# Performance work log

Hardware: AMD Instinct MI355X
Metric: run time of the kernel (lower is better)

## Reference

```python
import jax, jax.numpy as jnp
import numpy as np

NEG_SLOPE = 0.2   # negative_slope
EPS = 1e-6        # leaky-relu eps
BN_EPS = 1e-5     # torch BatchNorm default eps


def setup_inputs() -> dict:
    key = jax.random.key(0)
    k1, k2, k3 = jax.random.split(key, 3)
    B, C_in, C_out, N = 8, 256, 256, 8192
    x = jax.random.normal(k1, (B, C_in, 3, N), dtype=jnp.float32)
    s = 1.0 / np.sqrt(C_in)  # nn.Linear default init range
    W_feat = jax.random.uniform(k2, (C_out, C_in), minval=-s, maxval=s, dtype=jnp.float32)
    W_dir = jax.random.uniform(k3, (C_out, C_in), minval=-s, maxval=s, dtype=jnp.float32)
    gamma = jnp.ones((C_out,), jnp.float32)
    beta = jnp.zeros((C_out,), jnp.float32)
    return {"x": x, "W_feat": W_feat, "W_dir": W_dir, "gamma": gamma, "beta": beta}


def reference(x, W_feat, W_dir, gamma, beta):
    # VNLinear: kron(W, eye(3)) conv2d == per-vector channel mix
    p = jnp.einsum('oc,bcdn->bodn', W_feat, x)  # [B, O, 3, N]

    # VNBatchNorm: BN (training mode, batch stats) on vector norms, then rescale
    norm = jnp.sqrt(jnp.sum(p * p, axis=2))           # [B, O, N]
    mean = jnp.mean(norm, axis=(0, 2))                # [O]
    var = jnp.var(norm, axis=(0, 2))                  # [O] biased, as torch BN
    norm_bn = ((norm - mean[None, :, None]) * jax.lax.rsqrt(var + BN_EPS)[None, :, None]
               * gamma[None, :, None] + beta[None, :, None])
    p = p / norm[:, :, None, :] * norm_bn[:, :, None, :]

    # VNLeakyReLU with direction computed from the ORIGINAL input x
    d = jnp.einsum('oc,bcdn->bodn', W_dir, x)         # [B, O, 3, N]
    dot = jnp.sum(p * d, axis=2, keepdims=True)       # [B, O, 1, N]
    d_norm_sq = jnp.sum(d * d, axis=2, keepdims=True)
    return jnp.where(dot >= 0, p, p - (1.0 - NEG_SLOPE) * (dot / (d_norm_sq + EPS)) * d)
```

## Files before the change

kernel.cpp:

```cpp
#include <hip/hip_runtime.h>
#include <math.h>

#define BDIM 8
#define CIN  256
#define COUT 256
#define NDIM 8192

#define NEG_COEF  0.8f
#define LRELU_EPS 1e-6f
#define BN_EPS    1e-5f

typedef __attribute__((ext_vector_type(8))) short bf16x8;
typedef __attribute__((ext_vector_type(4))) float f32x4;

#define WS_WFH 0
#define WS_WFL 65536
#define WS_WDH 131072
#define WS_WDL 196608
#define WS_STATS_BYTE 524288
#define NSLOT 8

__device__ __forceinline__ unsigned short f2bf(float f) {
    unsigned u = __float_as_uint(f);
    return (unsigned short)((u + 0x7FFFu + ((u >> 16) & 1u)) >> 16);
}
__device__ __forceinline__ float bf2f(unsigned short h) {
    return __uint_as_float(((unsigned)h) << 16);
}

__global__ __launch_bounds__(256) void setup_w_kernel(
    const float* __restrict__ Wf, const float* __restrict__ Wd,
    unsigned short* __restrict__ wsu)
{
    const int o = blockIdx.x;
    const int mat = blockIdx.y;
    const int c = threadIdx.x;
    const float* W = mat ? Wd : Wf;
    float w = W[o * CIN + c];
    unsigned short hi = f2bf(w);
    unsigned short lo = f2bf(w - bf2f(hi));
    int pos = (c & ~31) + 4 * (c & 7) + ((c >> 3) & 3);
    unsigned short* ph = wsu + (mat ? WS_WDH : WS_WFH);
    unsigned short* pl = wsu + (mat ? WS_WDL : WS_WFL);
    ph[o * CIN + pos] = hi;
    pl[o * CIN + pos] = lo;
}

__global__ __launch_bounds__(256) void vn_stats_mfma(
    const float* __restrict__ x, const unsigned short* __restrict__ wsu,
    float* __restrict__ stats)
{
    __shared__ unsigned short sXhi[192 * 40];
    __shared__ float redS[64], redQ[64];

    const int t  = threadIdx.x;
    const int n0 = blockIdx.x * 64;
    const int o0 = blockIdx.y * 64;
    const int b  = blockIdx.z;

    const int lane = t & 63;
    const int w    = t >> 6;
    const int q    = lane >> 4;
    const int ln   = lane & 15;

    const int jl = t & 31;
    const int kb = t >> 5;

    if (t < 64) { redS[t] = 0.f; redQ[t] = 0.f; }

    f32x4 acc[2][6];
    #pragma unroll
    for (int i = 0; i < 2; ++i)
        #pragma unroll
        for (int j = 0; j < 6; ++j) acc[i][j] = (f32x4)0.f;

    const unsigned short* wfh = wsu + WS_WFH;
    const int oo = o0 + (w >> 1) * 32;
    const int nb = (w & 1) * 32;

    for (int c0 = 0; c0 < CIN; c0 += 32) {
        __syncthreads();
        #pragma unroll
        for (int ip = 0; ip < 6; ++ip) {
            int jloc = ip * 32 + jl;
            int d = jloc >> 6, nl = jloc & 63;
            float v[4];
            #pragma unroll
            for (int i = 0; i < 4; ++i) {
                int c = c0 + kb + 8 * i;
                v[i] = x[((size_t)((b * CIN + c) * 3 + d)) * NDIM + n0 + nl];
            }
            unsigned p0 = (unsigned)f2bf(v[0]) | ((unsigned)f2bf(v[1]) << 16);
            unsigned p1 = (unsigned)f2bf(v[2]) | ((unsigned)f2bf(v[3]) << 16);
            *(uint2*)&sXhi[jloc * 40 + kb * 4] = make_uint2(p0, p1);
        }
        __syncthreads();
        bf16x8 af[2];
        #pragma unroll
        for (int mt = 0; mt < 2; ++mt)
            af[mt] = *(const bf16x8*)&wfh[(oo + mt * 16 + ln) * CIN + c0 + q * 8];
        #pragma unroll
        for (int nt = 0; nt < 6; ++nt) {
            int d = nt >> 1, h = nt & 1;
            int jloc = d * 64 + nb + h * 16 + ln;
            bf16x8 bh = *(const bf16x8*)&sXhi[jloc * 40 + q * 8];
            #pragma unroll
            for (int mt = 0; mt < 2; ++mt)
                acc[mt][nt] = __builtin_amdgcn_mfma_f32_16x16x32_bf16(af[mt], bh, acc[mt][nt], 0, 0, 0);
        }
    }

    #pragma unroll
    for (int mt = 0; mt < 2; ++mt) {
        #pragma unroll
        for (int r = 0; r < 4; ++r) {
            float s = 0.f, s2 = 0.f;
            #pragma unroll
            for (int h = 0; h < 2; ++h) {
                float p0 = acc[mt][0 + h][r];
                float p1 = acc[mt][2 + h][r];
                float p2 = acc[mt][4 + h][r];
                float n2 = p0 * p0 + p1 * p1 + p2 * p2;
                s += sqrtf(n2); s2 += n2;
            }
            #pragma unroll
            for (int m = 1; m < 16; m <<= 1) {
                s  += __shfl_xor(s,  m, 64);
                s2 += __shfl_xor(s2, m, 64);
            }
            if (ln == 0) {
                int ol = (w >> 1) * 32 + mt * 16 + q * 4 + r;
                atomicAdd(&redS[ol], s);
                atomicAdd(&redQ[ol], s2);
            }
        }
    }
    __syncthreads();
    if (t < 64) {
        int slot = blockIdx.x & (NSLOT - 1);
        atomicAdd(&stats[slot * 256 + o0 + t], redS[t]);
        atomicAdd(&stats[NSLOT * 256 + slot * 256 + o0 + t], redQ[t]);
    }
}

__global__ __launch_bounds__(256) void vn_finalize2(
    float* __restrict__ stats, const float* __restrict__ gamma)
{
    int o = threadIdx.x;
    float s = 0.f, s2 = 0.f;
    #pragma unroll
    for (int i = 0; i < NSLOT; ++i) {
        s  += stats[i * 256 + o];
        s2 += stats[(NSLOT + i) * 256 + o];
    }
    const float inv = 1.0f / (float)(BDIM * NDIM);
    float mean = s * inv;
    float var  = fmaxf(s2 * inv - mean * mean, 0.f);
    stats[2 * NSLOT * 256 + o] = mean;
    stats[2 * NSLOT * 256 + 256 + o] = gamma[o] * rsqrtf(var + BN_EPS);
}

__global__ __launch_bounds__(256) void vn_main_mfma(
    const float* __restrict__ x, const unsigned short* __restrict__ wsu,
    const float* __restrict__ stats, const float* __restrict__ beta,
    float* __restrict__ out)
{
    __shared__ unsigned short sXhi[192 * 40];
    __shared__ unsigned short sXlo[192 * 40];

    const int t  = threadIdx.x;
    const int n0 = blockIdx.x * 64;
    const int o0 = blockIdx.y * 64;
    const int b  = blockIdx.z;

    const int lane = t & 63;
    const int w    = t >> 6;
    const int q    = lane >> 4;
    const int ln   = lane & 15;

    const int jl = t & 31;
    const int kb = t >> 5;

    f32x4 accP[2][6], accD[2][6];
    #pragma unroll
    for (int i = 0; i < 2; ++i)
        #pragma unroll
        for (int j = 0; j < 6; ++j) { accP[i][j] = (f32x4)0.f; accD[i][j] = (f32x4)0.f; }

    const unsigned short* wfh = wsu + WS_WFH;
    const unsigned short* wfl = wsu + WS_WFL;
    const unsigned short* wdh = wsu + WS_WDH;
    const unsigned short* wdl = wsu + WS_WDL;
    const int oo = o0 + (w >> 1) * 32;
    const int nb = (w & 1) * 32;

    for (int c0 = 0; c0 < CIN; c0 += 32) {
        __syncthreads();
        #pragma unroll
        for (int ip = 0; ip < 6; ++ip) {
            int jloc = ip * 32 + jl;
            int d = jloc >> 6, nl = jloc & 63;
            float v[4];
            #pragma unroll
            for (int i = 0; i < 4; ++i) {
                int c = c0 + kb + 8 * i;
                v[i] = x[((size_t)((b * CIN + c) * 3 + d)) * NDIM + n0 + nl];
            }
            unsigned short h0 = f2bf(v[0]), h1 = f2bf(v[1]), h2 = f2bf(v[2]), h3 = f2bf(v[3]);
            unsigned ph0 = (unsigned)h0 | ((unsigned)h1 << 16);
            unsigned ph1 = (unsigned)h2 | ((unsigned)h3 << 16);
            unsigned pl0 = (unsigned)f2bf(v[0] - bf2f(h0)) | ((unsigned)f2bf(v[1] - bf2f(h1)) << 16);
            unsigned pl1 = (unsigned)f2bf(v[2] - bf2f(h2)) | ((unsigned)f2bf(v[3] - bf2f(h3)) << 16);
            *(uint2*)&sXhi[jloc * 40 + kb * 4] = make_uint2(ph0, ph1);
            *(uint2*)&sXlo[jloc * 40 + kb * 4] = make_uint2(pl0, pl1);
        }
        __syncthreads();
        bf16x8 afh[2], afl[2], adh[2], adl[2];
        #pragma unroll
        for (int mt = 0; mt < 2; ++mt) {
            int row = (oo + mt * 16 + ln) * CIN + c0 + q * 8;
            afh[mt] = *(const bf16x8*)&wfh[row];
            afl[mt] = *(const bf16x8*)&wfl[row];
            adh[mt] = *(const bf16x8*)&wdh[row];
            adl[mt] = *(const bf16x8*)&wdl[row];
        }
        #pragma unroll
        for (int nt = 0; nt < 6; ++nt) {
            int d = nt >> 1, h = nt & 1;
            int jloc = d * 64 + nb + h * 16 + ln;
            bf16x8 bh = *(const bf16x8*)&sXhi[jloc * 40 + q * 8];
            bf16x8 bl = *(const bf16x8*)&sXlo[jloc * 40 + q * 8];
            #pragma unroll
            for (int mt = 0; mt < 2; ++mt) {
                f32x4 aP = accP[mt][nt];
                aP = __builtin_amdgcn_mfma_f32_16x16x32_bf16(afh[mt], bh, aP, 0, 0, 0);
                aP = __builtin_amdgcn_mfma_f32_16x16x32_bf16(afh[mt], bl, aP, 0, 0, 0);
                aP = __builtin_amdgcn_mfma_f32_16x16x32_bf16(afl[mt], bh, aP, 0, 0, 0);
                aP = __builtin_amdgcn_mfma_f32_16x16x32_bf16(afl[mt], bl, aP, 0, 0, 0);
                accP[mt][nt] = aP;
                f32x4 aD = accD[mt][nt];
                aD = __builtin_amdgcn_mfma_f32_16x16x32_bf16(adh[mt], bh, aD, 0, 0, 0);
                aD = __builtin_amdgcn_mfma_f32_16x16x32_bf16(adh[mt], bl, aD, 0, 0, 0);
                aD = __builtin_amdgcn_mfma_f32_16x16x32_bf16(adl[mt], bh, aD, 0, 0, 0);
                accD[mt][nt] = aD;
            }
        }
    }

    const float* meanp  = stats + 2 * NSLOT * 256;
    const float* scalep = meanp + 256;
    #pragma unroll
    for (int mt = 0; mt < 2; ++mt) {
        #pragma unroll
        for (int r = 0; r < 4; ++r) {
            const int o = oo + mt * 16 + q * 4 + r;
            const float mean  = meanp[o];
            const float scale = scalep[o];
            const float bet   = beta[o];
            #pragma unroll
            for (int h = 0; h < 2; ++h) {
                float p0 = accP[mt][0 + h][r], p1 = accP[mt][2 + h][r], p2 = accP[mt][4 + h][r];
                float d0 = accD[mt][0 + h][r], d1 = accD[mt][2 + h][r], d2 = accD[mt][4 + h][r];
                float n2 = p0 * p0 + p1 * p1 + p2 * p2;
                float nr = sqrtf(n2);
                float f  = ((nr - mean) * scale + bet) / nr;
                p0 *= f; p1 *= f; p2 *= f;
                float dot = p0 * d0 + p1 * d1 + p2 * d2;
                if (dot < 0.f) {
                    float g = NEG_COEF * dot / (d0 * d0 + d1 * d1 + d2 * d2 + LRELU_EPS);
                    p0 -= g * d0; p1 -= g * d1; p2 -= g * d2;
                }
                const int n = n0 + nb + h * 16 + ln;
                out[((size_t)(b * COUT + o) * 3 + 0) * NDIM + n] = p0;
                out[((size_t)(b * COUT + o) * 3 + 1) * NDIM + n] = p1;
                out[((size_t)(b * COUT + o) * 3 + 2) * NDIM + n] = p2;
            }
        }
    }
}

extern "C" void kernel_launch(void* const* d_in, const int* in_sizes, int n_in,
                              void* d_out, int out_size, void* d_ws, size_t ws_size,
                              hipStream_t stream) {
    const float* x     = (const float*)d_in[0];
    const float* Wf    = (const float*)d_in[1];
    const float* Wd    = (const float*)d_in[2];
    const float* gamma = (const float*)d_in[3];
    const float* beta  = (const float*)d_in[4];
    float* out = (float*)d_out;
    unsigned short* wsu = (unsigned short*)d_ws;
    float* stats = (float*)((char*)d_ws + WS_STATS_BYTE);

    hipMemsetAsync((char*)d_ws + WS_STATS_BYTE, 0, 2 * NSLOT * 256 * sizeof(float), stream);

    setup_w_kernel<<<dim3(256, 2), 256, 0, stream>>>(Wf, Wd, wsu);
    dim3 grid(NDIM / 64, COUT / 64, BDIM);
    vn_stats_mfma<<<grid, 256, 0, stream>>>(x, wsu, stats);
    vn_finalize2<<<1, 256, 0, stream>>>(stats, gamma);
    vn_main_mfma<<<grid, 256, 0, stream>>>(x, wsu, stats, beta, out);
}
```

Baseline: 601.4 us.

## Pre-convert x to swizzled bf16 hi/lo tiles in stats pass, reuse in main

The stats kernel now covers all 256 output channels per block (512 threads), so each x tile is read from fp32 and split into bf16 hi/lo only once. The swizzled tiles are written to a workspace image. The main kernel then loads these pre-split tiles directly into LDS with global_load_lds instead of re-reading fp32 x and redoing the split per output block. This removes three of the four redundant x reads and conversions in the stats pass, and all of them in the main pass. In exchange it writes and reads about 200 MB of extra workspace, and it falls back to the old path when the workspace is too small.

```diff
diff --git a/kernel.cpp b/kernel.cpp
--- a/kernel.cpp
+++ b/kernel.cpp
@@ -19,6 +19,11 @@
 #define WS_WDL 196608
 #define WS_STATS_BYTE 524288
 #define NSLOT 8
+#define TILE_BYTES 12288
+#define WS_XHI_BYTE 557056
+#define XIMG_BYTES 100663296ull
+#define WS_XLO_BYTE (WS_XHI_BYTE + XIMG_BYTES)
+#define WS_NEED (WS_XLO_BYTE + XIMG_BYTES)
 
 __device__ __forceinline__ unsigned short f2bf(float f) {
     unsigned u = __float_as_uint(f);
@@ -26,6 +31,16 @@
 }
 __device__ __forceinline__ float bf2f(unsigned short h) {
     return __uint_as_float(((unsigned)h) << 16);
+}
+
+__device__ __forceinline__ int swz(int off) {
+    return off ^ (((off >> 6) & 7) << 4);
+}
+
+__device__ __forceinline__ void gl_lds16(const char* g, char* l) {
+    __builtin_amdgcn_global_load_lds(
+        (const __attribute__((address_space(1))) unsigned int*)g,
+        (__attribute__((address_space(3))) unsigned int*)l, 16, 0, 0);
 }
 
 __global__ __launch_bounds__(256) void setup_w_kernel(
@@ -46,17 +61,21 @@
     pl[o * CIN + pos] = lo;
 }
 
-__global__ __launch_bounds__(256) void vn_stats_mfma(
+__global__ __launch_bounds__(512) void vn_statscvt(
     const float* __restrict__ x, const unsigned short* __restrict__ wsu,
+    char* __restrict__ xh, char* __restrict__ xl,
     float* __restrict__ stats)
 {
-    __shared__ unsigned short sXhi[192 * 40];
-    __shared__ float redS[64], redQ[64];
-
-    const int t  = threadIdx.x;
-    const int n0 = blockIdx.x * 64;
-    const int o0 = blockIdx.y * 64;
-    const int b  = blockIdx.z;
+    __shared__ uint4 sH4[TILE_BYTES / 16];
+    __shared__ uint4 sL4[TILE_BYTES / 16];
+    __shared__ float redS[256], redQ[256];
+    char* sH = (char*)sH4;
+    char* sL = (char*)sL4;
+
+    const int t    = threadIdx.x;
+    const int nblk = blockIdx.x;
+    const int b    = blockIdx.z;
+    const int n0   = nblk * 64;
 
     const int lane = t & 63;
     const int w    = t >> 6;
@@ -64,46 +83,64 @@
     const int ln   = lane & 15;
 
     const int jl = t & 31;
-    const int kb = t >> 5;
-
-    if (t < 64) { redS[t] = 0.f; redQ[t] = 0.f; }
-
-    f32x4 acc[2][6];
+    const int kb = (t >> 5) & 7;
+    const int u  = t >> 8;
+
+    if (t < 256) { redS[t] = 0.f; redQ[t] = 0.f; }
+
+    f32x4 acc[2][12];
     #pragma unroll
     for (int i = 0; i < 2; ++i)
         #pragma unroll
-        for (int j = 0; j < 6; ++j) acc[i][j] = (f32x4)0.f;
+        for (int j = 0; j < 12; ++j) acc[i][j] = (f32x4)0.f;
 
     const unsigned short* wfh = wsu + WS_WFH;
-    const int oo = o0 + (w >> 1) * 32;
-    const int nb = (w & 1) * 32;
-
-    for (int c0 = 0; c0 < CIN; c0 += 32) {
-        __syncthreads();
-        #pragma unroll
-        for (int ip = 0; ip < 6; ++ip) {
-            int jloc = ip * 32 + jl;
-            int d = jloc >> 6, nl = jloc & 63;
+    const int oo = w * 32;
+    char* ghb = xh + ((size_t)(b * 128 + nblk)) * (8 * TILE_BYTES);
+    char* glb = xl + ((size_t)(b * 128 + nblk)) * (8 * TILE_BYTES);
+
+    for (int ct = 0; ct < 8; ++ct) {
+        const int c0 = ct * 32;
+        __syncthreads();
+        #pragma unroll
+        for (int s = 0; s < 3; ++s) {
+            const int ip = u * 3 + s;
+            const int jloc = ip * 32 + jl;
+            const int d = jloc >> 6, nl = jloc & 63;
             float v[4];
             #pragma unroll
             for (int i = 0; i < 4; ++i) {
                 int c = c0 + kb + 8 * i;
                 v[i] = x[((size_t)((b * CIN + c) * 3 + d)) * NDIM + n0 + nl];
             }
-            unsigned p0 = (unsigned)f2bf(v[0]) | ((unsigned)f2bf(v[1]) << 16);
-            unsigned p1 = (unsigned)f2bf(v[2]) | ((unsigned)f2bf(v[3]) << 16);
-            *(uint2*)&sXhi[jloc * 40 + kb * 4] = make_uint2(p0, p1);
-        }
-        __syncthreads();
+            unsigned short h0 = f2bf(v[0]), h1 = f2bf(v[1]), h2 = f2bf(v[2]), h3 = f2bf(v[3]);
+            uint2 ph = make_uint2((unsigned)h0 | ((unsigned)h1 << 16),
+                                  (unsigned)h2 | ((unsigned)h3 << 16));
+            uint2 pl = make_uint2(
+                (unsigned)f2bf(v[0] - bf2f(h0)) | ((unsigned)f2bf(v[1] - bf2f(h1)) << 16),
+                (unsigned)f2bf(v[2] - bf2f(h2)) | ((unsigned)f2bf(v[3] - bf2f(h3)) << 16));
+            const int off = swz(jloc * 64 + kb * 8);
+            *(uint2*)(sH + off) = ph;
+            *(uint2*)(sL + off) = pl;
+        }
+        __syncthreads();
+        {
+            const int off = t * 48;
+            const char* src = (off < TILE_BYTES) ? (sH + off) : (sL + off - TILE_BYTES);
+            char* dst = (off < TILE_BYTES) ? (ghb + ct * TILE_BYTES + off)
+                                           : (glb + ct * TILE_BYTES + off - TILE_BYTES);
+            #pragma unroll
+            for (int p = 0; p < 3; ++p)
+                *(uint4*)(dst + p * 16) = *(const uint4*)(src + p * 16);
+        }
         bf16x8 af[2];
         #pragma unroll
         for (int mt = 0; mt < 2; ++mt)
             af[mt] = *(const bf16x8*)&wfh[(oo + mt * 16 + ln) * CIN + c0 + q * 8];
         #pragma unroll
-        for (int nt = 0; nt < 6; ++nt) {
-            int d = nt >> 1, h = nt & 1;
-            int jloc = d * 64 + nb + h * 16 + ln;
-            bf16x8 bh = *(const bf16x8*)&sXhi[jloc * 40 + q * 8];
+        for (int nt = 0; nt < 12; ++nt) {
+            const int jloc = nt * 16 + ln;
+            bf16x8 bh = *(const bf16x8*)(sH + swz(jloc * 64 + q * 16));
             #pragma unroll
             for (int mt = 0; mt < 2; ++mt)
                 acc[mt][nt] = __builtin_amdgcn_mfma_f32_16x16x32_bf16(af[mt], bh, acc[mt][nt], 0, 0, 0);
@@ -116,10 +153,10 @@
         for (int r = 0; r < 4; ++r) {
             float s = 0.f, s2 = 0.f;
             #pragma unroll
-            for (int h = 0; h < 2; ++h) {
+            for (int h = 0; h < 4; ++h) {
                 float p0 = acc[mt][0 + h][r];
-                float p1 = acc[mt][2 + h][r];
-                float p2 = acc[mt][4 + h][r];
+                float p1 = acc[mt][4 + h][r];
+                float p2 = acc[mt][8 + h][r];
                 float n2 = p0 * p0 + p1 * p1 + p2 * p2;
                 s += sqrtf(n2); s2 += n2;
             }
@@ -129,17 +166,17 @@
                 s2 += __shfl_xor(s2, m, 64);
             }
             if (ln == 0) {
-                int ol = (w >> 1) * 32 + mt * 16 + q * 4 + r;
-                atomicAdd(&redS[ol], s);
-                atomicAdd(&redQ[ol], s2);
+                int o = oo + mt * 16 + q * 4 + r;
+                atomicAdd(&redS[o], s);
+                atomicAdd(&redQ[o], s2);
             }
         }
     }
     __syncthreads();
-    if (t < 64) {
-        int slot = blockIdx.x & (NSLOT - 1);
-        atomicAdd(&stats[slot * 256 + o0 + t], redS[t]);
-        atomicAdd(&stats[NSLOT * 256 + slot * 256 + o0 + t], redQ[t]);
+    if (t < 256) {
+        int slot = nblk & (NSLOT - 1);
+        atomicAdd(&stats[slot * 256 + t], redS[t]);
+        atomicAdd(&stats[NSLOT * 256 + slot * 256 + t], redQ[t]);
     }
 }
 
@@ -160,26 +197,27 @@
     stats[2 * NSLOT * 256 + 256 + o] = gamma[o] * rsqrtf(var + BN_EPS);
 }
 
-__global__ __launch_bounds__(256) void vn_main_mfma(
-    const float* __restrict__ x, const unsigned short* __restrict__ wsu,
+__global__ __launch_bounds__(256) void vn_main2(
+    const unsigned short* __restrict__ wsu,
+    const char* __restrict__ xh, const char* __restrict__ xl,
     const float* __restrict__ stats, const float* __restrict__ beta,
     float* __restrict__ out)
 {
-    __shared__ unsigned short sXhi[192 * 40];
-    __shared__ unsigned short sXlo[192 * 40];
-
-    const int t  = threadIdx.x;
-    const int n0 = blockIdx.x * 64;
-    const int o0 = blockIdx.y * 64;
-    const int b  = blockIdx.z;
+    __shared__ uint4 sH4[TILE_BYTES / 16];
+    __shared__ uint4 sL4[TILE_BYTES / 16];
+    char* sH = (char*)sH4;
+    char* sL = (char*)sL4;
+
+    const int t    = threadIdx.x;
+    const int nblk = blockIdx.x;
+    const int n0   = nblk * 64;
+    const int o0   = blockIdx.y * 64;
+    const int b    = blockIdx.z;
 
     const int lane = t & 63;
     const int w    = t >> 6;
     const int q    = lane >> 4;
     const int ln   = lane & 15;
-
-    const int jl = t & 31;
-    const int kb = t >> 5;
 
     f32x4 accP[2][6], accD[2][6];
     #pragma unroll
@@ -194,31 +232,23 @@
     const int oo = o0 + (w >> 1) * 32;
     const int nb = (w & 1) * 32;
 
-    for (int c0 = 0; c0 < CIN; c0 += 32) {
-        __syncthreads();
-        #pragma unroll
-        for (int ip = 0; ip < 6; ++ip) {
-            int jloc = ip * 32 + jl;
-            int d = jloc >> 6, nl = jloc & 63;
-            float v[4];
-            #pragma unroll
-            for (int i = 0; i < 4; ++i) {
-                int c = c0 + kb + 8 * i;
-                v[i] = x[((size_t)((b * CIN + c) * 3 + d)) * NDIM + n0 + nl];
-            }
-            unsigned short h0 = f2bf(v[0]), h1 = f2bf(v[1]), h2 = f2bf(v[2]), h3 = f2bf(v[3]);
-            unsigned ph0 = (unsigned)h0 | ((unsigned)h1 << 16);
-            unsigned ph1 = (unsigned)h2 | ((unsigned)h3 << 16);
-            unsigned pl0 = (unsigned)f2bf(v[0] - bf2f(h0)) | ((unsigned)f2bf(v[1] - bf2f(h1)) << 16);
-            unsigned pl1 = (unsigned)f2bf(v[2] - bf2f(h2)) | ((unsigned)f2bf(v[3] - bf2f(h3)) << 16);
-            *(uint2*)&sXhi[jloc * 40 + kb * 4] = make_uint2(ph0, ph1);
-            *(uint2*)&sXlo[jloc * 40 + kb * 4] = make_uint2(pl0, pl1);
-        }
-        __syncthreads();
+    const char* ghb = xh + ((size_t)(b * 128 + nblk)) * (8 * TILE_BYTES);
+    const char* glb = xl + ((size_t)(b * 128 + nblk)) * (8 * TILE_BYTES);
+
+    for (int ct = 0; ct < 8; ++ct) {
+        __syncthreads();
+        #pragma unroll
+        for (int p = 0; p < 3; ++p) {
+            gl_lds16(ghb + ct * TILE_BYTES + t * 16 + p * 4096, sH + t * 16 + p * 4096);
+            gl_lds16(glb + ct * TILE_BYTES + t * 16 + p * 4096, sL + t * 16 + p * 4096);
+        }
+        __syncthreads();
+
+        const int c0 = ct * 32;
         bf16x8 afh[2], afl[2], adh[2], adl[2];
         #pragma unroll
         for (int mt = 0; mt < 2; ++mt) {
-            int row = (oo + mt * 16 + ln) * CIN + c0 + q * 8;
+            const int row = (oo + mt * 16 + ln) * CIN + c0 + q * 8;
             afh[mt] = *(const bf16x8*)&wfh[row];
             afl[mt] = *(const bf16x8*)&wfl[row];
             adh[mt] = *(const bf16x8*)&wdh[row];
@@ -226,10 +256,11 @@
         }
         #pragma unroll
         for (int nt = 0; nt < 6; ++nt) {
-            int d = nt >> 1, h = nt & 1;
-            int jloc = d * 64 + nb + h * 16 + ln;
-            bf16x8 bh = *(const bf16x8*)&sXhi[jloc * 40 + q * 8];
-            bf16x8 bl = *(const bf16x8*)&sXlo[jloc * 40 + q * 8];
+            const int d = nt >> 1, h = nt & 1;
+            const int jloc = d * 64 + nb + h * 16 + ln;
+            const int off = swz(jloc * 64 + q * 16);
+            bf16x8 bh = *(const bf16x8*)(sH + off);
+            bf16x8 bl = *(const bf16x8*)(sL + off);
             #pragma unroll
             for (int mt = 0; mt < 2; ++mt) {
                 f32x4 aP = accP[mt][nt];
@@ -279,6 +310,222 @@
     }
 }
 
+__global__ __launch_bounds__(256) void vn_stats_mfma(
+    const float* __restrict__ x, const unsigned short* __restrict__ wsu,
+    float* __restrict__ stats)
+{
+    __shared__ unsigned short sXhi[192 * 40];
+    __shared__ float redS[64], redQ[64];
+
+    const int t  = threadIdx.x;
+    const int n0 = blockIdx.x * 64;
+    const int o0 = blockIdx.y * 64;
+    const int b  = blockIdx.z;
+
+    const int lane = t & 63;
+    const int w    = t >> 6;
+    const int q    = lane >> 4;
+    const int ln   = lane & 15;
+
+    const int jl = t & 31;
+    const int kb = t >> 5;
+
+    if (t < 64) { redS[t] = 0.f; redQ[t] = 0.f; }
+
+    f32x4 acc[2][6];
+    #pragma unroll
+    for (int i = 0; i < 2; ++i)
+        #pragma unroll
+        for (int j = 0; j < 6; ++j) acc[i][j] = (f32x4)0.f;
+
+    const unsigned short* wfh = wsu + WS_WFH;
+    const int oo = o0 + (w >> 1) * 32;
+    const int nb = (w & 1) * 32;
+
+    for (int c0 = 0; c0 < CIN; c0 += 32) {
+        __syncthreads();
+        #pragma unroll
+        for (int ip = 0; ip < 6; ++ip) {
+            int jloc = ip * 32 + jl;
+            int d = jloc >> 6, nl = jloc & 63;
+            float v[4];
+            #pragma unroll
+            for (int i = 0; i < 4; ++i) {
+                int c = c0 + kb + 8 * i;
+                v[i] = x[((size_t)((b * CIN + c) * 3 + d)) * NDIM + n0 + nl];
+            }
+            unsigned p0 = (unsigned)f2bf(v[0]) | ((unsigned)f2bf(v[1]) << 16);
+            unsigned p1 = (unsigned)f2bf(v[2]) | ((unsigned)f2bf(v[3]) << 16);
+            *(uint2*)&sXhi[jloc * 40 + kb * 4] = make_uint2(p0, p1);
+        }
+        __syncthreads();
+        bf16x8 af[2];
+        #pragma unroll
+        for (int mt = 0; mt < 2; ++mt)
+            af[mt] = *(const bf16x8*)&wfh[(oo + mt * 16 + ln) * CIN + c0 + q * 8];
+        #pragma unroll
+        for (int nt = 0; nt < 6; ++nt) {
+            int d = nt >> 1, h = nt & 1;
+            int jloc = d * 64 + nb + h * 16 + ln;
+            bf16x8 bh = *(const bf16x8*)&sXhi[jloc * 40 + q * 8];
+            #pragma unroll
+            for (int mt = 0; mt < 2; ++mt)
+                acc[mt][nt] = __builtin_amdgcn_mfma_f32_16x16x32_bf16(af[mt], bh, acc[mt][nt], 0, 0, 0);
+        }
+    }
+
+    #pragma unroll
+    for (int mt = 0; mt < 2; ++mt) {
+        #pragma unroll
+        for (int r = 0; r < 4; ++r) {
+            float s = 0.f, s2 = 0.f;
+            #pragma unroll
+            for (int h = 0; h < 2; ++h) {
+                float p0 = acc[mt][0 + h][r];
+                float p1 = acc[mt][2 + h][r];
+                float p2 = acc[mt][4 + h][r];
+                float n2 = p0 * p0 + p1 * p1 + p2 * p2;
+                s += sqrtf(n2); s2 += n2;
+            }
+            #pragma unroll
+            for (int m = 1; m < 16; m <<= 1) {
+                s  += __shfl_xor(s,  m, 64);
+                s2 += __shfl_xor(s2, m, 64);
+            }
+            if (ln == 0) {
+                int ol = (w >> 1) * 32 + mt * 16 + q * 4 + r;
+                atomicAdd(&redS[ol], s);
+                atomicAdd(&redQ[ol], s2);
+            }
+        }
+    }
+    __syncthreads();
+    if (t < 64) {
+        int slot = blockIdx.x & (NSLOT - 1);
+        atomicAdd(&stats[slot * 256 + o0 + t], redS[t]);
+        atomicAdd(&stats[NSLOT * 256 + slot * 256 + o0 + t], redQ[t]);
+    }
+}
+
+__global__ __launch_bounds__(256) void vn_main_mfma(
+    const float* __restrict__ x, const unsigned short* __restrict__ wsu,
+    const float* __restrict__ stats, const float* __restrict__ beta,
+    float* __restrict__ out)
+{
+    __shared__ unsigned short sXhi[192 * 40];
+    __shared__ unsigned short sXlo[192 * 40];
+
+    const int t  = threadIdx.x;
+    const int n0 = blockIdx.x * 64;
+    const int o0 = blockIdx.y * 64;
+    const int b  = blockIdx.z;
+
+    const int lane = t & 63;
+    const int w    = t >> 6;
+    const int q    = lane >> 4;
+    const int ln   = lane & 15;
+
+    const int jl = t & 31;
+    const int kb = t >> 5;
+
+    f32x4 accP[2][6], accD[2][6];
+    #pragma unroll
+    for (int i = 0; i < 2; ++i)
+        #pragma unroll
+        for (int j = 0; j < 6; ++j) { accP[i][j] = (f32x4)0.f; accD[i][j] = (f32x4)0.f; }
+
+    const unsigned short* wfh = wsu + WS_WFH;
+    const unsigned short* wfl = wsu + WS_WFL;
+    const unsigned short* wdh = wsu + WS_WDH;
+    const unsigned short* wdl = wsu + WS_WDL;
+    const int oo = o0 + (w >> 1) * 32;
+    const int nb = (w & 1) * 32;
+
+    for (int c0 = 0; c0 < CIN; c0 += 32) {
+        __syncthreads();
+        #pragma unroll
+        for (int ip = 0; ip < 6; ++ip) {
+            int jloc = ip * 32 + jl;
+            int d = jloc >> 6, nl = jloc & 63;
+            float v[4];
+            #pragma unroll
+            for (int i = 0; i < 4; ++i) {
+                int c = c0 + kb + 8 * i;
+                v[i] = x[((size_t)((b * CIN + c) * 3 + d)) * NDIM + n0 + nl];
+            }
+            unsigned short h0 = f2bf(v[0]), h1 = f2bf(v[1]), h2 = f2bf(v[2]), h3 = f2bf(v[3]);
+            unsigned ph0 = (unsigned)h0 | ((unsigned)h1 << 16);
+            unsigned ph1 = (unsigned)h2 | ((unsigned)h3 << 16);
+            unsigned pl0 = (unsigned)f2bf(v[0] - bf2f(h0)) | ((unsigned)f2bf(v[1] - bf2f(h1)) << 16);
+            unsigned pl1 = (unsigned)f2bf(v[2] - bf2f(h2)) | ((unsigned)f2bf(v[3] - bf2f(h3)) << 16);
+            *(uint2*)&sXhi[jloc * 40 + kb * 4] = make_uint2(ph0, ph1);
+            *(uint2*)&sXlo[jloc * 40 + kb * 4] = make_uint2(pl0, pl1);
+        }
+        __syncthreads();
+        bf16x8 afh[2], afl[2], adh[2], adl[2];
+        #pragma unroll
+        for (int mt = 0; mt < 2; ++mt) {
+            int row = (oo + mt * 16 + ln) * CIN + c0 + q * 8;
+            afh[mt] = *(const bf16x8*)&wfh[row];
+            afl[mt] = *(const bf16x8*)&wfl[row];
+            adh[mt] = *(const bf16x8*)&wdh[row];
+            adl[mt] = *(const bf16x8*)&wdl[row];
+        }
+        #pragma unroll
+        for (int nt = 0; nt < 6; ++nt) {
+            int d = nt >> 1, h = nt & 1;
+            int jloc = d * 64 + nb + h * 16 + ln;
+            bf16x8 bh = *(const bf16x8*)&sXhi[jloc * 40 + q * 8];
+            bf16x8 bl = *(const bf16x8*)&sXlo[jloc * 40 + q * 8];
+            #pragma unroll
+            for (int mt = 0; mt < 2; ++mt) {
+                f32x4 aP = accP[mt][nt];
+                aP = __builtin_amdgcn_mfma_f32_16x16x32_bf16(afh[mt], bh, aP, 0, 0, 0);
+                aP = __builtin_amdgcn_mfma_f32_16x16x32_bf16(afh[mt], bl, aP, 0, 0, 0);
+                aP = __builtin_amdgcn_mfma_f32_16x16x32_bf16(afl[mt], bh, aP, 0, 0, 0);
+                aP = __builtin_amdgcn_mfma_f32_16x16x32_bf16(afl[mt], bl, aP, 0, 0, 0);
+                accP[mt][nt] = aP;
+                f32x4 aD = accD[mt][nt];
+                aD = __builtin_amdgcn_mfma_f32_16x16x32_bf16(adh[mt], bh, aD, 0, 0, 0);
+                aD = __builtin_amdgcn_mfma_f32_16x16x32_bf16(adh[mt], bl, aD, 0, 0, 0);
+                aD = __builtin_amdgcn_mfma_f32_16x16x32_bf16(adl[mt], bh, aD, 0, 0, 0);
+                accD[mt][nt] = aD;
+            }
+        }
+    }
+
+    const float* meanp  = stats + 2 * NSLOT * 256;
+    const float* scalep = meanp + 256;
+    #pragma unroll
+    for (int mt = 0; mt < 2; ++mt) {
+        #pragma unroll
+        for (int r = 0; r < 4; ++r) {
+            const int o = oo + mt * 16 + q * 4 + r;
+            const float mean  = meanp[o];
+            const float scale = scalep[o];
+            const float bet   = beta[o];
+            #pragma unroll
+            for (int h = 0; h < 2; ++h) {
+                float p0 = accP[mt][0 + h][r], p1 = accP[mt][2 + h][r], p2 = accP[mt][4 + h][r];
+                float d0 = accD[mt][0 + h][r], d1 = accD[mt][2 + h][r], d2 = accD[mt][4 + h][r];
+                float n2 = p0 * p0 + p1 * p1 + p2 * p2;
+                float nr = sqrtf(n2);
+                float f  = ((nr - mean) * scale + bet) / nr;
+                p0 *= f; p1 *= f; p2 *= f;
+                float dot = p0 * d0 + p1 * d1 + p2 * d2;
+                if (dot < 0.f) {
+                    float g = NEG_COEF * dot / (d0 * d0 + d1 * d1 + d2 * d2 + LRELU_EPS);
+                    p0 -= g * d0; p1 -= g * d1; p2 -= g * d2;
+                }
+                const int n = n0 + nb + h * 16 + ln;
+                out[((size_t)(b * COUT + o) * 3 + 0) * NDIM + n] = p0;
+                out[((size_t)(b * COUT + o) * 3 + 1) * NDIM + n] = p1;
+                out[((size_t)(b * COUT + o) * 3 + 2) * NDIM + n] = p2;
+            }
+        }
+    }
+}
+
 extern "C" void kernel_launch(void* const* d_in, const int* in_sizes, int n_in,
                               void* d_out, int out_size, void* d_ws, size_t ws_size,
                               hipStream_t stream) {
@@ -292,10 +539,18 @@
     float* stats = (float*)((char*)d_ws + WS_STATS_BYTE);
 
     hipMemsetAsync((char*)d_ws + WS_STATS_BYTE, 0, 2 * NSLOT * 256 * sizeof(float), stream);
-
     setup_w_kernel<<<dim3(256, 2), 256, 0, stream>>>(Wf, Wd, wsu);
-    dim3 grid(NDIM / 64, COUT / 64, BDIM);
-    vn_stats_mfma<<<grid, 256, 0, stream>>>(x, wsu, stats);
-    vn_finalize2<<<1, 256, 0, stream>>>(stats, gamma);
-    vn_main_mfma<<<grid, 256, 0, stream>>>(x, wsu, stats, beta, out);
-}
+
+    if (ws_size >= (size_t)WS_NEED) {
+        char* xhp = (char*)d_ws + WS_XHI_BYTE;
+        char* xlp = (char*)d_ws + WS_XLO_BYTE;
+        vn_statscvt<<<dim3(128, 1, 8), 512, 0, stream>>>(x, wsu, xhp, xlp, stats);
+        vn_finalize2<<<1, 256, 0, stream>>>(stats, gamma);
+        vn_main2<<<dim3(128, 4, 8), 256, 0, stream>>>(wsu, xhp, xlp, stats, beta, out);
+    } else {
+        dim3 grid(NDIM / 64, COUT / 64, BDIM);
+        vn_stats_mfma<<<grid, 256, 0, stream>>>(x, wsu, stats);
+        vn_finalize2<<<1, 256, 0, stream>>>(stats, gamma);
+        vn_main_mfma<<<grid, 256, 0, stream>>>(x, wsu, stats, beta, out);
+    }
+}
```

Result: slower. 708.4 us (+17.8%).
